# Kernel tuning notes

Measured on AMD Instinct MI355X. Metric: run time of the kernel, lower is better.

## Reference

```python
import jax, jax.numpy as jnp
import numpy as np

SUB_NO = 64
SYN_BASIS_NO = 3
T_HIST = 200
T_DATA = 100000


def setup_inputs() -> dict:
    key = jax.random.key(0)
    ks = jax.random.split(key, 5)
    # strictly-lower-triangular adjacency: each subunit integrates from ancestors
    C_den = jnp.tril((jax.random.uniform(ks[0], (SUB_NO, SUB_NO)) < 0.15).astype(jnp.float32), k=-1)
    S_conv = jax.random.normal(ks[1], (T_DATA, SUB_NO), dtype=jnp.float32)
    Y_ancest = 0.1 * jax.random.normal(ks[2], (T_DATA, SUB_NO), dtype=jnp.float32)
    # sparse binary spike trains
    Z_ancest = (jax.random.uniform(ks[3], (T_DATA, SUB_NO)) < 0.05).astype(jnp.float32)
    V_o = jnp.full((1,), -69.0, dtype=jnp.float32)
    W_sub = jnp.full((SUB_NO,), 0.25, dtype=jnp.float32)
    theta_syn = jnp.zeros((SUB_NO,), dtype=jnp.float32)
    K_spike = jnp.full((SUB_NO, SYN_BASIS_NO), 0.01, dtype=jnp.float32)
    tau_spike = jnp.arange(1.6, 1.6 + SYN_BASIS_NO, dtype=jnp.float32)
    delta_spike = jnp.zeros((SUB_NO,), dtype=jnp.float32)
    return {"S_conv": S_conv, "Y_ancest": Y_ancest, "Z_ancest": Z_ancest,
            "C_den": C_den, "V_o": V_o, "W_sub": W_sub, "theta_syn": theta_syn,
            "K_spike": K_spike, "tau_spike": tau_spike, "delta_spike": delta_spike,
            "T_hist": T_HIST}


def _ancest_kernel(K_spike, tau_spike, delta_spike, T_hist):
    # t[s, k] = max(k - delta_s, 0); kern[s, k] = sum_b (t/tau_b) exp(-t/tau_b) K[s,b]
    t = jnp.arange(T_hist, dtype=jnp.float32)[None, :] - delta_spike[:, None]
    t = jnp.maximum(t, 0.0)                                  # [sub, T_hist]
    tau = jnp.exp(tau_spike)                                 # [basis]
    t_tau = t[:, None, :] / tau[None, :, None]               # [sub, basis, T_hist]
    kern = jnp.sum(t_tau * jnp.exp(-t_tau) * K_spike[:, :, None], axis=1)
    return kern                                              # [sub, T_hist]


def reference(S_conv, Y_ancest, Z_ancest, C_den, V_o, W_sub, theta_syn,
              K_spike, tau_spike, delta_spike, T_hist):
    T_data, sub_no = S_conv.shape
    kern = _ancest_kernel(K_spike, tau_spike, delta_spike, T_hist)
    kern_f = jnp.flip(kern, axis=1)                          # matches torch.flip

    # spike_ancest[t, s, k] = sum_j C_den[s,j] Z_pad[t+k, j]  ->  precontract once
    Zc = Z_ancest @ C_den.T                                  # [T, sub]
    Zc_pad = jnp.concatenate([jnp.zeros((T_hist, sub_no), Zc.dtype), Zc], axis=0)
    # depthwise VALID conv over time: filtered[t, s] = sum_k kern_f[s,k] Zc_pad[t+k, s]
    out = jax.lax.conv_general_dilated(
        Zc_pad.T[None],                                      # [1, sub, T+T_hist]
        kern_f[:, None, :],                                  # [sub, 1, T_hist]
        window_strides=(1,), padding='VALID',
        feature_group_count=sub_no,
        dimension_numbers=('NCH', 'OIH', 'NCH'))
    filtered = out[0, :, :T_data].T                          # [T, sub]

    raw = Y_ancest @ C_den.T                                 # [T, sub]
    X_in = S_conv + theta_syn + filtered + raw
    final_Y = jax.nn.sigmoid(X_in) * W_sub + V_o
    return final_Y
```

## Files before the change

kernel.cpp:

```cpp
#include <hip/hip_runtime.h>

#define SUBS  64
#define GUARD 256
#define LB    32
#define JT    8
#define LSTR  136

typedef _Float16 f16x8 __attribute__((ext_vector_type(8)));
typedef float    f32x4 __attribute__((ext_vector_type(4)));

union uh2 { uint u; _Float16 h[2]; };

__device__ inline f16x8 ld_frag(const float* p) {
    float4 a = *(const float4*)p;
    float4 b = *(const float4*)(p + 4);
    f16x8 f;
    f[0]=(_Float16)a.x; f[1]=(_Float16)a.y; f[2]=(_Float16)a.z; f[3]=(_Float16)a.w;
    f[4]=(_Float16)b.x; f[5]=(_Float16)b.y; f[6]=(_Float16)b.z; f[7]=(_Float16)b.w;
    return f;
}
__device__ inline uint pkh2(float a, float b) {
    union { _Float16 h[2]; uint u; } p;
    p.h[0] = (_Float16)a; p.h[1] = (_Float16)b; return p.u;
}

#define STEP3(u)                                                                 \
    _Pragma("unroll")                                                            \
    for (int b = 0; b < 3; ++b) {                                                \
        const float yn = fmaf(twr[b], y1[b], fmaf(mr2[b], y2[b], cr[b] * (u)));  \
        y2[b] = y1[b]; y1[b] = yn;                                               \
    }
#define PAIRW(wrd) {                                                             \
    uh2 w_; w_.u = (wrd);                                                        \
    STEP3((float)w_.h[0]);                                                       \
    STEP3((float)w_.h[1]); }

__global__ __launch_bounds__(256, 4) void k_mm(
    const float* __restrict__ Z, const float* __restrict__ Y,
    const float* __restrict__ C,
    const float* __restrict__ K_spike, const float* __restrict__ tau_spike,
    const float* __restrict__ delta_spike,
    _Float16* __restrict__ Zt, _Float16* __restrict__ Yt,
    float* __restrict__ fb, int T, int rgz, int NB)
{
    __shared__ _Float16 ztl[SUBS * LSTR];
    __shared__ _Float16 ytl[SUBS * LSTR];
    const int tid  = threadIdx.x;
    const int lane = tid & 63;
    const int wv   = tid >> 6;
    const int lr   = lane & 15;
    const int lg   = lane >> 4;
    const int t0b  = blockIdx.x * 128;

    int dl = (int)rintf(delta_spike[lane]);
    dl = min(max(dl, 0), 30);
    const bool alldl0 = __all(dl == 0);

    if (blockIdx.x == 0) {
        for (int idx = tid; idx < JT * 512; idx += 256) fb[idx] = 0.f;
    }
    if (!alldl0) {
        if (blockIdx.x < 8) {
            const int tile = blockIdx.x * 4 + wv;
            uint4 z4 = {0, 0, 0, 0};
            ((uint4*)Zt)[(size_t)tile * 64 + lane] = z4;
            ((uint4*)Yt)[(size_t)tile * 64 + lane] = z4;
        } else if (blockIdx.x < 18) {
            const int tile = rgz + (blockIdx.x - 8) * 4 + wv;
            uint4 z4 = {0, 0, 0, 0};
            ((uint4*)Zt)[(size_t)tile * 64 + lane] = z4;
            ((uint4*)Yt)[(size_t)tile * 64 + lane] = z4;
        }
    }

    f16x8 bfr[4][2];
    #pragma unroll
    for (int nt = 0; nt < 4; ++nt)
        #pragma unroll
        for (int ks = 0; ks < 2; ++ks)
            bfr[nt][ks] = ld_frag(&C[(lr + 16 * nt) * 64 + ks * 32 + lg * 8]);

    #pragma unroll
    for (int g = 0; g < 2; ++g) {
        const int t0 = t0b + wv * 32 + g * 16;
        const int rowA = t0 + lr;
        const bool okA = rowA < T;
        f16x8 az[2], ay[2];
        #pragma unroll
        for (int ks = 0; ks < 2; ++ks) {
            if (okA) {
                az[ks] = ld_frag(&Z[(size_t)rowA * 64 + ks * 32 + lg * 8]);
                ay[ks] = ld_frag(&Y[(size_t)rowA * 64 + ks * 32 + lg * 8]);
            } else {
                az[ks] = (f16x8)(_Float16)0.f;
                ay[ks] = (f16x8)(_Float16)0.f;
            }
        }

        f32x4 accZ[4], accY[4];
        #pragma unroll
        for (int nt = 0; nt < 4; ++nt) { accZ[nt] = (f32x4){0,0,0,0}; accY[nt] = (f32x4){0,0,0,0}; }
        #pragma unroll
        for (int nt = 0; nt < 4; ++nt) {
            #pragma unroll
            for (int ks = 0; ks < 2; ++ks) {
                accZ[nt] = __builtin_amdgcn_mfma_f32_16x16x32_f16(az[ks], bfr[nt][ks], accZ[nt], 0, 0, 0);
                accY[nt] = __builtin_amdgcn_mfma_f32_16x16x32_f16(ay[ks], bfr[nt][ks], accY[nt], 0, 0, 0);
            }
        }

        #pragma unroll
        for (int nt = 0; nt < 4; ++nt) {
            const int sc = lr + 16 * nt;
            const int lt = wv * 32 + g * 16 + lg * 4;
            uint2 pz, py;
            pz.x = pkh2(accZ[nt][0], accZ[nt][1]);
            pz.y = pkh2(accZ[nt][2], accZ[nt][3]);
            py.x = pkh2(accY[nt][0], accY[nt][1]);
            py.y = pkh2(accY[nt][2], accY[nt][3]);
            *(uint2*)&ztl[sc * LSTR + lt] = pz;
            *(uint2*)&ytl[sc * LSTR + lt] = py;
        }
    }

    __syncthreads();

    const int grun = blockIdx.x * 4 + wv;
    if (grun < NB) {
        float twr[3], mr2[3], cr[3];
        #pragma unroll
        for (int b = 0; b < 3; ++b) {
            const float tau = __expf(tau_spike[b]);
            const float r   = __expf(-1.0f / tau);
            twr[b] = 2.0f * r;
            mr2[b] = -r * r;
            cr[b]  = K_spike[lane * 3 + b] / tau * r;
        }
        const uint* zr = (const uint*)ztl + lane * (LSTR / 2) + wv * 16;
        float y1[3] = {0.f, 0.f, 0.f}, y2[3] = {0.f, 0.f, 0.f};
        #pragma unroll
        for (int k = 0; k < 16; ++k) PAIRW(zr[k]);
        float* fout = fb + (size_t)(grun + JT) * 512 + lane * 8;
        *(float4*)fout       = make_float4(y1[0], y2[0], y1[1], y2[1]);
        *(float2*)(fout + 4) = make_float2(y1[2], y2[2]);
    }

    const int gbase = (GUARD >> 3) + blockIdx.x * 16;
    #pragma unroll
    for (int it = 0; it < 4; ++it) {
        const int chunk = it * 256 + tid;
        const int row = chunk & 63;
        const int col = chunk >> 6;
        const int tb  = t0b + col * 8;
        if (tb + 7 < T) {
            ((uint4*)Zt)[(size_t)(gbase + col) * 64 + row] =
                *(const uint4*)&ztl[row * LSTR + col * 8];
            ((uint4*)Yt)[(size_t)(gbase + col) * 64 + row] =
                *(const uint4*)&ytl[row * LSTR + col * 8];
        } else {
            union { ushort u[8]; uint4 v; } vz, vy;
            #pragma unroll
            for (int h = 0; h < 8; ++h) {
                const bool ok = (tb + h < T);
                vz.u[h] = ok ? ((const ushort*)ztl)[row * LSTR + col * 8 + h] : (ushort)0;
                vy.u[h] = ok ? ((const ushort*)ytl)[row * LSTR + col * 8 + h] : (ushort)0;
            }
            ((uint4*)Zt)[(size_t)(gbase + col) * 64 + row] = vz.v;
            ((uint4*)Yt)[(size_t)(gbase + col) * 64 + row] = vy.v;
        }
    }
}

#define OUTP(o, yh, ph, f) {                                                     \
    const int t_ = t0 + (o);                                                     \
    if (t_ < T) {                                                                \
        const float xin_ = (float)(yh) + (float)(ph) + (f);                      \
        const float sig_ = 1.0f / (1.0f + __expf(-xin_));                        \
        out[(size_t)t_ * 64 + s] = fmaf(sig_, wsub, vo);                         \
    } }

#define PW(xwrd, ywrd, swrd, ob) {                                               \
    uh2 wx_, wy_, wp_;                                                           \
    wx_.u = (xwrd); wy_.u = (ywrd); wp_.u = (swrd);                              \
    STEP3((float)wx_.h[0]);                                                      \
    OUTP((ob),     wy_.h[0], wp_.h[0], y1[0] + y1[1] + y1[2]);                   \
    STEP3((float)wx_.h[1]);                                                      \
    OUTP((ob) + 1, wy_.h[1], wp_.h[1], y1[0] + y1[1] + y1[2]); }

__global__ __launch_bounds__(256, 3) void k_iir2(
    const _Float16* __restrict__ Zt, const _Float16* __restrict__ Yt,
    const float* __restrict__ S,
    const float* __restrict__ K_spike, const float* __restrict__ tau_spike,
    const float* __restrict__ delta_spike, const float* __restrict__ theta,
    const float* __restrict__ W, const float* __restrict__ Vo,
    const float* __restrict__ fb, float* __restrict__ out, int T, int NB)
{
    const int tid = threadIdx.x;
    const int s   = tid & 63;
    const int wv  = tid >> 6;
    const int i   = blockIdx.x * 4 + wv;
    if (i >= NB) return;
    const int t0 = i * LB;

    float twr[3], mr2[3], cr[3], taus[3];
    #pragma unroll
    for (int b = 0; b < 3; ++b) {
        const float tau = __expf(tau_spike[b]);
        taus[b] = tau;
        const float r = __expf(-1.0f / tau);
        twr[b] = 2.0f * r;
        mr2[b] = -r * r;
        cr[b]  = K_spike[s * 3 + b] / tau * r;
    }
    int dl = (int)rintf(delta_spike[s]);
    dl = min(max(dl, 0), 30);
    const float th   = theta[s];
    const float wsub = W[s];
    const float vo   = Vo[0];

    if (__all(dl == 0) && (t0 + LB <= T)) {
        const float* spp = S + (size_t)t0 * 64 + s;
        uint4 sp0, sp1, sp2, sp3;
        sp0.x = pkh2(spp[   0] + th, spp[  64] + th);
        sp0.y = pkh2(spp[ 128] + th, spp[ 192] + th);
        sp0.z = pkh2(spp[ 256] + th, spp[ 320] + th);
        sp0.w = pkh2(spp[ 384] + th, spp[ 448] + th);
        sp1.x = pkh2(spp[ 512] + th, spp[ 576] + th);
        sp1.y = pkh2(spp[ 640] + th, spp[ 704] + th);
        sp1.z = pkh2(spp[ 768] + th, spp[ 832] + th);
        sp1.w = pkh2(spp[ 896] + th, spp[ 960] + th);
        sp2.x = pkh2(spp[1024] + th, spp[1088] + th);
        sp2.y = pkh2(spp[1152] + th, spp[1216] + th);
        sp2.z = pkh2(spp[1280] + th, spp[1344] + th);
        sp2.w = pkh2(spp[1408] + th, spp[1472] + th);
        sp3.x = pkh2(spp[1536] + th, spp[1600] + th);
        sp3.y = pkh2(spp[1664] + th, spp[1728] + th);
        sp3.z = pkh2(spp[1792] + th, spp[1856] + th);
        sp3.w = pkh2(spp[1920] + th, spp[1984] + th);

        float aL[3], bL[3], cL[3], dL[3];
        #pragma unroll
        for (int b = 0; b < 3; ++b) {
            const float r   = 0.5f * twr[b];
            const float rm1 = __expf(-(float)(LB - 1) / taus[b]);
            const float rl  = rm1 * r;
            const float rp  = rl * r;
            aL[b] = (float)(LB + 1) * rl;
            bL[b] = -(float)LB * rp;
            cL[b] = (float)LB * rm1;
            dL[b] = -(float)(LB - 1) * rl;
        }
        float y1[3], y2[3];
        {
            const float* fq = fb + (size_t)i * 512 + s * 8;
            const float4 lo = *(const float4*)fq;
            const float2 hi = *(const float2*)(fq + 4);
            y1[0] = lo.x; y2[0] = lo.y; y1[1] = lo.z; y2[1] = lo.w;
            y1[2] = hi.x; y2[2] = hi.y;
        }
        #pragma unroll
        for (int j = 7; j >= 1; --j) {
            const float* fq = fb + (size_t)(i + JT - j) * 512 + s * 8;
            const float4 lo = *(const float4*)fq;
            const float2 hi = *(const float2*)(fq + 4);
            float n1, n2;
            n1 = fmaf(aL[0], y1[0], fmaf(bL[0], y2[0], lo.x));
            n2 = fmaf(cL[0], y1[0], fmaf(dL[0], y2[0], lo.y));
            y1[0] = n1; y2[0] = n2;
            n1 = fmaf(aL[1], y1[1], fmaf(bL[1], y2[1], lo.z));
            n2 = fmaf(cL[1], y1[1], fmaf(dL[1], y2[1], lo.w));
            y1[1] = n1; y2[1] = n2;
            n1 = fmaf(aL[2], y1[2], fmaf(bL[2], y2[2], hi.x));
            n2 = fmaf(cL[2], y1[2], fmaf(dL[2], y2[2], hi.y));
            y1[2] = n1; y2[2] = n2;
        }

        const uint4* xb = (const uint4*)Zt + (size_t)(32 + 4 * i) * 64 + s;
        const uint4 x0 = xb[0], x1 = xb[64], x2 = xb[128], x3 = xb[192];
        const uint4* yb = (const uint4*)Yt + (size_t)(32 + 4 * i) * 64 + s;
        const uint4 yv0 = yb[0], yv1 = yb[64], yv2 = yb[128], yv3 = yb[192];

        {
            uh2 wy_, wp_;
            wy_.u = yv0.x; wp_.u = sp0.x;
            OUTP(0, wy_.h[0], wp_.h[0], y2[0] + y2[1] + y2[2]);
            OUTP(1, wy_.h[1], wp_.h[1], y1[0] + y1[1] + y1[2]);
        }
        PW(x0.x, yv0.y, sp0.y,  2);  PW(x0.y, yv0.z, sp0.z,  4);
        PW(x0.z, yv0.w, sp0.w,  6);  PW(x0.w, yv1.x, sp1.x,  8);
        PW(x1.x, yv1.y, sp1.y, 10);  PW(x1.y, yv1.z, sp1.z, 12);
        PW(x1.z, yv1.w, sp1.w, 14);  PW(x1.w, yv2.x, sp2.x, 16);
        PW(x2.x, yv2.y, sp2.y, 18);  PW(x2.y, yv2.z, sp2.z, 20);
        PW(x2.z, yv2.w, sp2.w, 22);  PW(x2.w, yv3.x, sp3.x, 24);
        PW(x3.x, yv3.y, sp3.y, 26);  PW(x3.y, yv3.z, sp3.z, 28);
        PW(x3.z, yv3.w, sp3.w, 30);
    } else {
        float y1[3] = {0.f, 0.f, 0.f}, y2[3] = {0.f, 0.f, 0.f};
        const int xi0 = t0 - 226 - dl;
        for (int k = 0; k < 224 + LB; ++k) {
            const int h = GUARD + xi0 + k;
            const float u = (float)Zt[(size_t)(h >> 3) * 512 + s * 8 + (h & 7)];
            STEP3(u);
            const int o = k - 224;
            if (o >= 0) {
                const int t = t0 + o;
                if (t < T) {
                    const int hy = GUARD + t;
                    const float yc = (float)Yt[(size_t)(hy >> 3) * 512 + s * 8 + (hy & 7)];
                    const float xin = yc + S[(size_t)t * 64 + s] + th
                                      + y1[0] + y1[1] + y1[2];
                    const float sig = 1.0f / (1.0f + __expf(-xin));
                    out[(size_t)t * 64 + s] = fmaf(sig, wsub, vo);
                }
            }
        }
    }
}

extern "C" void kernel_launch(void* const* d_in, const int* in_sizes, int n_in,
                              void* d_out, int out_size, void* d_ws, size_t ws_size,
                              hipStream_t stream)
{
    const float* S     = (const float*)d_in[0];
    const float* Y     = (const float*)d_in[1];
    const float* Z     = (const float*)d_in[2];
    const float* C     = (const float*)d_in[3];
    const float* Vo    = (const float*)d_in[4];
    const float* W     = (const float*)d_in[5];
    const float* theta = (const float*)d_in[6];
    const float* K     = (const float*)d_in[7];
    const float* tau   = (const float*)d_in[8];
    const float* delta = (const float*)d_in[9];
    const int T  = in_sizes[0] / SUBS;
    const int NB = (T + LB - 1) / LB;

    const int rgz    = (GUARD + T + 7) >> 3;
    const int ntiles = rgz + 44;
    _Float16* Zt = (_Float16*)d_ws;
    _Float16* Yt = (_Float16*)((char*)d_ws + (size_t)ntiles * 1024);
    float*    fb = (float*)((char*)d_ws + (size_t)ntiles * 2048);

    k_mm<<<(T + 127) / 128, 256, 0, stream>>>(Z, Y, C, K, tau, delta,
                                              Zt, Yt, fb, T, rgz, NB);
    k_iir2<<<(NB + 3) / 4, 256, 0, stream>>>(Zt, Yt, S, K, tau, delta, theta,
                                             W, Vo, fb, (float*)d_out, T, NB);
}
```

Baseline: 47.64 us.

## Split sigmoid epilogue into separate vectorized kernel with fp16 intermediate

```diff
diff --git a/kernel.cpp b/kernel.cpp
--- a/kernel.cpp
+++ b/kernel.cpp
@@ -171,29 +171,24 @@
     }
 }
 
-#define OUTP(o, yh, ph, f) {                                                     \
+#define PREW(o, yh, f) {                                                         \
     const int t_ = t0 + (o);                                                     \
-    if (t_ < T) {                                                                \
-        const float xin_ = (float)(yh) + (float)(ph) + (f);                      \
-        const float sig_ = 1.0f / (1.0f + __expf(-xin_));                        \
-        out[(size_t)t_ * 64 + s] = fmaf(sig_, wsub, vo);                         \
-    } }
-
-#define PW(xwrd, ywrd, swrd, ob) {                                               \
-    uh2 wx_, wy_, wp_;                                                           \
-    wx_.u = (xwrd); wy_.u = (ywrd); wp_.u = (swrd);                              \
+    if (t_ < T) pre[(size_t)t_ * 64 + s] = (_Float16)((float)(yh) + (f));        \
+    }
+
+#define PW(xwrd, ywrd, ob) {                                                     \
+    uh2 wx_, wy_;                                                                \
+    wx_.u = (xwrd); wy_.u = (ywrd);                                              \
     STEP3((float)wx_.h[0]);                                                      \
-    OUTP((ob),     wy_.h[0], wp_.h[0], y1[0] + y1[1] + y1[2]);                   \
+    PREW((ob),     wy_.h[0], y1[0] + y1[1] + y1[2]);                             \
     STEP3((float)wx_.h[1]);                                                      \
-    OUTP((ob) + 1, wy_.h[1], wp_.h[1], y1[0] + y1[1] + y1[2]); }
-
-__global__ __launch_bounds__(256, 3) void k_iir2(
+    PREW((ob) + 1, wy_.h[1], y1[0] + y1[1] + y1[2]); }
+
+__global__ __launch_bounds__(256, 4) void k_iir2(
     const _Float16* __restrict__ Zt, const _Float16* __restrict__ Yt,
-    const float* __restrict__ S,
     const float* __restrict__ K_spike, const float* __restrict__ tau_spike,
-    const float* __restrict__ delta_spike, const float* __restrict__ theta,
-    const float* __restrict__ W, const float* __restrict__ Vo,
-    const float* __restrict__ fb, float* __restrict__ out, int T, int NB)
+    const float* __restrict__ delta_spike,
+    const float* __restrict__ fb, _Float16* __restrict__ pre, int T, int NB)
 {
     const int tid = threadIdx.x;
     const int s   = tid & 63;
@@ -214,30 +209,8 @@
     }
     int dl = (int)rintf(delta_spike[s]);
     dl = min(max(dl, 0), 30);
-    const float th   = theta[s];
-    const float wsub = W[s];
-    const float vo   = Vo[0];
 
     if (__all(dl == 0) && (t0 + LB <= T)) {
-        const float* spp = S + (size_t)t0 * 64 + s;
-        uint4 sp0, sp1, sp2, sp3;
-        sp0.x = pkh2(spp[   0] + th, spp[  64] + th);
-        sp0.y = pkh2(spp[ 128] + th, spp[ 192] + th);
-        sp0.z = pkh2(spp[ 256] + th, spp[ 320] + th);
-        sp0.w = pkh2(spp[ 384] + th, spp[ 448] + th);
-        sp1.x = pkh2(spp[ 512] + th, spp[ 576] + th);
-        sp1.y = pkh2(spp[ 640] + th, spp[ 704] + th);
-        sp1.z = pkh2(spp[ 768] + th, spp[ 832] + th);
-        sp1.w = pkh2(spp[ 896] + th, spp[ 960] + th);
-        sp2.x = pkh2(spp[1024] + th, spp[1088] + th);
-        sp2.y = pkh2(spp[1152] + th, spp[1216] + th);
-        sp2.z = pkh2(spp[1280] + th, spp[1344] + th);
-        sp2.w = pkh2(spp[1408] + th, spp[1472] + th);
-        sp3.x = pkh2(spp[1536] + th, spp[1600] + th);
-        sp3.y = pkh2(spp[1664] + th, spp[1728] + th);
-        sp3.z = pkh2(spp[1792] + th, spp[1856] + th);
-        sp3.w = pkh2(spp[1920] + th, spp[1984] + th);
-
         float aL[3], bL[3], cL[3], dL[3];
         #pragma unroll
         for (int b = 0; b < 3; ++b) {
@@ -281,19 +254,18 @@
         const uint4 yv0 = yb[0], yv1 = yb[64], yv2 = yb[128], yv3 = yb[192];
 
         {
-            uh2 wy_, wp_;
-            wy_.u = yv0.x; wp_.u = sp0.x;
-            OUTP(0, wy_.h[0], wp_.h[0], y2[0] + y2[1] + y2[2]);
-            OUTP(1, wy_.h[1], wp_.h[1], y1[0] + y1[1] + y1[2]);
-        }
-        PW(x0.x, yv0.y, sp0.y,  2);  PW(x0.y, yv0.z, sp0.z,  4);
-        PW(x0.z, yv0.w, sp0.w,  6);  PW(x0.w, yv1.x, sp1.x,  8);
-        PW(x1.x, yv1.y, sp1.y, 10);  PW(x1.y, yv1.z, sp1.z, 12);
-        PW(x1.z, yv1.w, sp1.w, 14);  PW(x1.w, yv2.x, sp2.x, 16);
-        PW(x2.x, yv2.y, sp2.y, 18);  PW(x2.y, yv2.z, sp2.z, 20);
-        PW(x2.z, yv2.w, sp2.w, 22);  PW(x2.w, yv3.x, sp3.x, 24);
-        PW(x3.x, yv3.y, sp3.y, 26);  PW(x3.y, yv3.z, sp3.z, 28);
-        PW(x3.z, yv3.w, sp3.w, 30);
+            uh2 wy_; wy_.u = yv0.x;
+            PREW(0, wy_.h[0], y2[0] + y2[1] + y2[2]);
+            PREW(1, wy_.h[1], y1[0] + y1[1] + y1[2]);
+        }
+        PW(x0.x, yv0.y,  2);  PW(x0.y, yv0.z,  4);
+        PW(x0.z, yv0.w,  6);  PW(x0.w, yv1.x,  8);
+        PW(x1.x, yv1.y, 10);  PW(x1.y, yv1.z, 12);
+        PW(x1.z, yv1.w, 14);  PW(x1.w, yv2.x, 16);
+        PW(x2.x, yv2.y, 18);  PW(x2.y, yv2.z, 20);
+        PW(x2.z, yv2.w, 22);  PW(x2.w, yv3.x, 24);
+        PW(x3.x, yv3.y, 26);  PW(x3.y, yv3.z, 28);
+        PW(x3.z, yv3.w, 30);
     } else {
         float y1[3] = {0.f, 0.f, 0.f}, y2[3] = {0.f, 0.f, 0.f};
         const int xi0 = t0 - 226 - dl;
@@ -307,13 +279,53 @@
                 if (t < T) {
                     const int hy = GUARD + t;
                     const float yc = (float)Yt[(size_t)(hy >> 3) * 512 + s * 8 + (hy & 7)];
-                    const float xin = yc + S[(size_t)t * 64 + s] + th
-                                      + y1[0] + y1[1] + y1[2];
-                    const float sig = 1.0f / (1.0f + __expf(-xin));
-                    out[(size_t)t * 64 + s] = fmaf(sig, wsub, vo);
+                    pre[(size_t)t * 64 + s] = (_Float16)(yc + y1[0] + y1[1] + y1[2]);
                 }
             }
         }
+    }
+}
+
+__global__ __launch_bounds__(256) void k_sig(
+    const _Float16* __restrict__ pre, const float* __restrict__ S,
+    const float* __restrict__ theta, const float* __restrict__ W,
+    const float* __restrict__ Vo, float* __restrict__ out, int n8)
+{
+    __shared__ float wls[SUBS], tls[SUBS];
+    if (threadIdx.x < SUBS) {
+        wls[threadIdx.x] = W[threadIdx.x];
+        tls[threadIdx.x] = theta[threadIdx.x];
+    }
+    __syncthreads();
+    const float vo = Vo[0];
+
+    for (int c = blockIdx.x * 256 + threadIdx.x; c < n8; c += gridDim.x * 256) {
+        const size_t base = (size_t)c * 8;
+        const uint4  pv = *(const uint4*)(pre + base);
+        const float4 s0 = *(const float4*)(S + base);
+        const float4 s1 = *(const float4*)(S + base + 4);
+        const int sb = (int)(base & 63);
+
+        uh2 p0, p1, p2, p3;
+        p0.u = pv.x; p1.u = pv.y; p2.u = pv.z; p3.u = pv.w;
+
+        float4 o0, o1;
+        #define SIG1(ph, sv, thj, wj, dst) {                                     \
+            const float xin = (float)(ph) + (sv) + tls[sb + (thj)];              \
+            const float sg  = 1.0f / (1.0f + __expf(-xin));                      \
+            dst = fmaf(sg, wls[sb + (wj)], vo); }
+        SIG1(p0.h[0], s0.x, 0, 0, o0.x);
+        SIG1(p0.h[1], s0.y, 1, 1, o0.y);
+        SIG1(p1.h[0], s0.z, 2, 2, o0.z);
+        SIG1(p1.h[1], s0.w, 3, 3, o0.w);
+        SIG1(p2.h[0], s1.x, 4, 4, o1.x);
+        SIG1(p2.h[1], s1.y, 5, 5, o1.y);
+        SIG1(p3.h[0], s1.z, 6, 6, o1.z);
+        SIG1(p3.h[1], s1.w, 7, 7, o1.w);
+        #undef SIG1
+
+        *(float4*)(out + base)     = o0;
+        *(float4*)(out + base + 4) = o1;
     }
 }
 
@@ -336,12 +348,15 @@
 
     const int rgz    = (GUARD + T + 7) >> 3;
     const int ntiles = rgz + 44;
-    _Float16* Zt = (_Float16*)d_ws;
-    _Float16* Yt = (_Float16*)((char*)d_ws + (size_t)ntiles * 1024);
-    float*    fb = (float*)((char*)d_ws + (size_t)ntiles * 2048);
+    _Float16* Zt  = (_Float16*)d_ws;
+    _Float16* Yt  = (_Float16*)((char*)d_ws + (size_t)ntiles * 1024);
+    float*    fb  = (float*)((char*)d_ws + (size_t)ntiles * 2048);
+    _Float16* pre = (_Float16*)((char*)d_ws + (size_t)ntiles * 2048
+                                + (size_t)(NB + JT + 4) * 2048);
 
     k_mm<<<(T + 127) / 128, 256, 0, stream>>>(Z, Y, C, K, tau, delta,
                                               Zt, Yt, fb, T, rgz, NB);
-    k_iir2<<<(NB + 3) / 4, 256, 0, stream>>>(Zt, Yt, S, K, tau, delta, theta,
-                                             W, Vo, fb, (float*)d_out, T, NB);
-}
+    k_iir2<<<(NB + 3) / 4, 256, 0, stream>>>(Zt, Yt, K, tau, delta, fb, pre, T, NB);
+    const int n8 = (T * SUBS) / 8;
+    k_sig<<<2048, 256, 0, stream>>>(pre, S, theta, W, Vo, (float*)d_out, n8);
+}
```

Measured after the change: 50.81 us. 1.07x slower.

## Split each 32-step IIR block into two 16-step halves per wavefront

Applied to the files above, without the earlier changes.

```diff
diff --git a/kernel.cpp b/kernel.cpp
--- a/kernel.cpp
+++ b/kernel.cpp
@@ -41,7 +41,7 @@
     const float* __restrict__ K_spike, const float* __restrict__ tau_spike,
     const float* __restrict__ delta_spike,
     _Float16* __restrict__ Zt, _Float16* __restrict__ Yt,
-    float* __restrict__ fb, int T, int rgz, int NB)
+    float* __restrict__ fb, float* __restrict__ gb, int T, int rgz, int NB)
 {
     __shared__ _Float16 ztl[SUBS * LSTR];
     __shared__ _Float16 ytl[SUBS * LSTR];
@@ -139,7 +139,12 @@
         const uint* zr = (const uint*)ztl + lane * (LSTR / 2) + wv * 16;
         float y1[3] = {0.f, 0.f, 0.f}, y2[3] = {0.f, 0.f, 0.f};
         #pragma unroll
-        for (int k = 0; k < 16; ++k) PAIRW(zr[k]);
+        for (int k = 0; k < 8; ++k) PAIRW(zr[k]);
+        float* gout = gb + (size_t)grun * 512 + lane * 8;
+        *(float4*)gout       = make_float4(y1[0], y2[0], y1[1], y2[1]);
+        *(float2*)(gout + 4) = make_float2(y1[2], y2[2]);
+        #pragma unroll
+        for (int k = 8; k < 16; ++k) PAIRW(zr[k]);
         float* fout = fb + (size_t)(grun + JT) * 512 + lane * 8;
         *(float4*)fout       = make_float4(y1[0], y2[0], y1[1], y2[1]);
         *(float2*)(fout + 4) = make_float2(y1[2], y2[2]);
@@ -193,14 +198,17 @@
     const float* __restrict__ K_spike, const float* __restrict__ tau_spike,
     const float* __restrict__ delta_spike, const float* __restrict__ theta,
     const float* __restrict__ W, const float* __restrict__ Vo,
-    const float* __restrict__ fb, float* __restrict__ out, int T, int NB)
+    const float* __restrict__ fb, const float* __restrict__ gb,
+    float* __restrict__ out, int T, int NB)
 {
     const int tid = threadIdx.x;
     const int s   = tid & 63;
     const int wv  = tid >> 6;
-    const int i   = blockIdx.x * 4 + wv;
+    const int gid = blockIdx.x * 4 + wv;
+    const int i   = gid >> 1;
+    const int hf  = gid & 1;
     if (i >= NB) return;
-    const int t0 = i * LB;
+    const int t0 = i * LB + 16 * hf;
 
     float twr[3], mr2[3], cr[3], taus[3];
     #pragma unroll
@@ -218,25 +226,23 @@
     const float wsub = W[s];
     const float vo   = Vo[0];
 
-    if (__all(dl == 0) && (t0 + LB <= T)) {
+    if (__all(dl == 0) && ((i + 1) * LB <= T)) {
+        const int tb = 32 + 4 * i + 2 * hf;
+        const uint4* xb = (const uint4*)Zt + (size_t)tb * 64 + s;
+        const uint4 xA = xb[0], xB = xb[64];
+        const uint4* yb = (const uint4*)Yt + (size_t)tb * 64 + s;
+        const uint4 yA = yb[0], yB = yb[64];
+
         const float* spp = S + (size_t)t0 * 64 + s;
-        uint4 sp0, sp1, sp2, sp3;
-        sp0.x = pkh2(spp[   0] + th, spp[  64] + th);
-        sp0.y = pkh2(spp[ 128] + th, spp[ 192] + th);
-        sp0.z = pkh2(spp[ 256] + th, spp[ 320] + th);
-        sp0.w = pkh2(spp[ 384] + th, spp[ 448] + th);
-        sp1.x = pkh2(spp[ 512] + th, spp[ 576] + th);
-        sp1.y = pkh2(spp[ 640] + th, spp[ 704] + th);
-        sp1.z = pkh2(spp[ 768] + th, spp[ 832] + th);
-        sp1.w = pkh2(spp[ 896] + th, spp[ 960] + th);
-        sp2.x = pkh2(spp[1024] + th, spp[1088] + th);
-        sp2.y = pkh2(spp[1152] + th, spp[1216] + th);
-        sp2.z = pkh2(spp[1280] + th, spp[1344] + th);
-        sp2.w = pkh2(spp[1408] + th, spp[1472] + th);
-        sp3.x = pkh2(spp[1536] + th, spp[1600] + th);
-        sp3.y = pkh2(spp[1664] + th, spp[1728] + th);
-        sp3.z = pkh2(spp[1792] + th, spp[1856] + th);
-        sp3.w = pkh2(spp[1920] + th, spp[1984] + th);
+        uint4 spA, spB;
+        spA.x = pkh2(spp[  0] + th, spp[ 64] + th);
+        spA.y = pkh2(spp[128] + th, spp[192] + th);
+        spA.z = pkh2(spp[256] + th, spp[320] + th);
+        spA.w = pkh2(spp[384] + th, spp[448] + th);
+        spB.x = pkh2(spp[512] + th, spp[576] + th);
+        spB.y = pkh2(spp[640] + th, spp[704] + th);
+        spB.z = pkh2(spp[768] + th, spp[832] + th);
+        spB.w = pkh2(spp[896] + th, spp[960] + th);
 
         float aL[3], bL[3], cL[3], dL[3];
         #pragma unroll
@@ -275,35 +281,47 @@
             y1[2] = n1; y2[2] = n2;
         }
 
-        const uint4* xb = (const uint4*)Zt + (size_t)(32 + 4 * i) * 64 + s;
-        const uint4 x0 = xb[0], x1 = xb[64], x2 = xb[128], x3 = xb[192];
-        const uint4* yb = (const uint4*)Yt + (size_t)(32 + 4 * i) * 64 + s;
-        const uint4 yv0 = yb[0], yv1 = yb[64], yv2 = yb[128], yv3 = yb[192];
+        if (hf) {
+            const float* gq = gb + (size_t)i * 512 + s * 8;
+            const float4 glo = *(const float4*)gq;
+            const float2 ghi = *(const float2*)(gq + 4);
+            const float g1[3] = { glo.x, glo.z, ghi.x };
+            const float g2[3] = { glo.y, glo.w, ghi.y };
+            #pragma unroll
+            for (int b = 0; b < 3; ++b) {
+                const float r   = 0.5f * twr[b];
+                const float r15 = __expf(-15.0f / taus[b]);
+                const float r16 = r15 * r;
+                const float r17 = r16 * r;
+                const float n1 = fmaf(17.0f * r16, y1[b],
+                                 fmaf(-16.0f * r17, y2[b], g1[b]));
+                const float n2 = fmaf(16.0f * r15, y1[b],
+                                 fmaf(-15.0f * r16, y2[b], g2[b]));
+                y1[b] = n1; y2[b] = n2;
+            }
+        }
 
         {
             uh2 wy_, wp_;
-            wy_.u = yv0.x; wp_.u = sp0.x;
+            wy_.u = yA.x; wp_.u = spA.x;
             OUTP(0, wy_.h[0], wp_.h[0], y2[0] + y2[1] + y2[2]);
             OUTP(1, wy_.h[1], wp_.h[1], y1[0] + y1[1] + y1[2]);
         }
-        PW(x0.x, yv0.y, sp0.y,  2);  PW(x0.y, yv0.z, sp0.z,  4);
-        PW(x0.z, yv0.w, sp0.w,  6);  PW(x0.w, yv1.x, sp1.x,  8);
-        PW(x1.x, yv1.y, sp1.y, 10);  PW(x1.y, yv1.z, sp1.z, 12);
-        PW(x1.z, yv1.w, sp1.w, 14);  PW(x1.w, yv2.x, sp2.x, 16);
-        PW(x2.x, yv2.y, sp2.y, 18);  PW(x2.y, yv2.z, sp2.z, 20);
-        PW(x2.z, yv2.w, sp2.w, 22);  PW(x2.w, yv3.x, sp3.x, 24);
-        PW(x3.x, yv3.y, sp3.y, 26);  PW(x3.y, yv3.z, sp3.z, 28);
-        PW(x3.z, yv3.w, sp3.w, 30);
-    } else {
+        PW(xA.x, yA.y, spA.y,  2);  PW(xA.y, yA.z, spA.z,  4);
+        PW(xA.z, yA.w, spA.w,  6);  PW(xA.w, yB.x, spB.x,  8);
+        PW(xB.x, yB.y, spB.y, 10);  PW(xB.y, yB.z, spB.z, 12);
+        PW(xB.z, yB.w, spB.w, 14);
+    } else if (hf == 0) {
         float y1[3] = {0.f, 0.f, 0.f}, y2[3] = {0.f, 0.f, 0.f};
-        const int xi0 = t0 - 226 - dl;
+        const int bt0 = i * LB;
+        const int xi0 = bt0 - 226 - dl;
         for (int k = 0; k < 224 + LB; ++k) {
             const int h = GUARD + xi0 + k;
             const float u = (float)Zt[(size_t)(h >> 3) * 512 + s * 8 + (h & 7)];
             STEP3(u);
             const int o = k - 224;
             if (o >= 0) {
-                const int t = t0 + o;
+                const int t = bt0 + o;
                 if (t < T) {
                     const int hy = GUARD + t;
                     const float yc = (float)Yt[(size_t)(hy >> 3) * 512 + s * 8 + (hy & 7)];
@@ -339,9 +357,12 @@
     _Float16* Zt = (_Float16*)d_ws;
     _Float16* Yt = (_Float16*)((char*)d_ws + (size_t)ntiles * 1024);
     float*    fb = (float*)((char*)d_ws + (size_t)ntiles * 2048);
+    float*    gb = (float*)((char*)d_ws + (size_t)ntiles * 2048
+                            + (size_t)(NB + JT + 4) * 2048);
 
     k_mm<<<(T + 127) / 128, 256, 0, stream>>>(Z, Y, C, K, tau, delta,
-                                              Zt, Yt, fb, T, rgz, NB);
-    k_iir2<<<(NB + 3) / 4, 256, 0, stream>>>(Zt, Yt, S, K, tau, delta, theta,
-                                             W, Vo, fb, (float*)d_out, T, NB);
-}
+                                              Zt, Yt, fb, gb, T, rgz, NB);
+    k_iir2<<<(2 * NB + 3) / 4, 256, 0, stream>>>(Zt, Yt, S, K, tau, delta, theta,
+                                                 W, Vo, fb, gb,
+                                                 (float*)d_out, T, NB);
+}
```

Measured after the change: 48.46 us. About the same (+1.7%).
